# Kernel tuning notes

Hardware: AMD Instinct MI355X
Metric: run time of the kernel (lower is better)

Reference implementation:

```python
import jax, jax.numpy as jnp
import numpy as np
from jax import lax

NUM_CLASSES = 80
NUM_ANCHORS = 5
INPUT_SIZE = 1280
LAYER = 40  # INPUT_SIZE / 32
CONF_T = 0.5
IOU_T = 0.45
ANCHORS = np.array([[1.3221, 1.73145], [3.19275, 4.00944], [5.05587, 8.09892],
                    [9.47112, 4.84053], [11.2364, 10.0071]], dtype=np.float32)


def setup_inputs() -> dict:
    key = jax.random.key(0)
    x = jax.random.normal(key, (1, NUM_ANCHORS * (5 + NUM_CLASSES), LAYER, LAYER), dtype=jnp.float32)
    return {"x": x, "scaled_anchors": jnp.asarray(ANCHORS)}


def _decode(x, anchors):
    # x: (1, A*(5+C), H, W) -> boxes (N,4) in input_size scale, conf (N,), cls (N,)
    b, _, H, W = x.shape
    A = anchors.shape[0]
    stride_w = INPUT_SIZE / W
    stride_h = INPUT_SIZE / H
    pred = x.reshape(b, A, 5 + NUM_CLASSES, H, W).transpose(0, 1, 3, 4, 2)  # (b,A,H,W,5+C)
    gx, gy = jnp.meshgrid(jnp.arange(W, dtype=x.dtype), jnp.arange(H, dtype=x.dtype))
    grid = jnp.stack([gx, gy], axis=-1)  # (H,W,2)
    pxy = jax.nn.sigmoid(pred[..., 0:2]) + grid  # (b,A,H,W,2)
    pwh = jnp.exp(pred[..., 2:4]) * anchors[None, :, None, None, :]
    stride = jnp.array([stride_w, stride_h, stride_w, stride_h], dtype=x.dtype)
    pbox = jnp.concatenate([pxy, pwh], axis=-1) * stride  # (b,A,H,W,4)
    pconf = jax.nn.sigmoid(pred[..., 4])
    # sigmoid is monotonic so argmax over sigmoid(logits) == argmax over logits
    pcls = jnp.argmax(pred[..., 5:], axis=-1)
    N = A * H * W
    return pbox.reshape(N, 4), pconf.reshape(N), pcls.reshape(N)


def _nms_keep(boxes, conf, cls):
    # Greedy per-class NMS; returns fixed-shape boolean keep mask of shape (N,)
    N = boxes.shape[0]
    valid = conf > CONF_T
    cx, cy, w, h = boxes[:, 0], boxes[:, 1], boxes[:, 2], boxes[:, 3]
    x1, y1, x2, y2 = cx - w / 2, cy - h / 2, cx + w / 2, cy + h / 2
    area = jnp.maximum(x2 - x1, 0.0) * jnp.maximum(y2 - y1, 0.0)
    ix1 = jnp.maximum(x1[:, None], x1[None, :])
    iy1 = jnp.maximum(y1[:, None], y1[None, :])
    ix2 = jnp.minimum(x2[:, None], x2[None, :])
    iy2 = jnp.minimum(y2[:, None], y2[None, :])
    inter = jnp.maximum(ix2 - ix1, 0.0) * jnp.maximum(iy2 - iy1, 0.0)
    iou = inter / (area[:, None] + area[None, :] - inter + 1e-9)  # (N,N)

    score = jnp.where(valid, conf, -1.0)
    order = jnp.argsort(-score)

    def step(carry, idx):
        keep, sup = carry
        active = valid[idx] & ~sup[idx]
        keep = keep.at[idx].set(active)
        row = (iou[idx] > IOU_T) & (cls == cls[idx])
        sup = sup | (active & row)
        return (keep, sup), None

    init = (jnp.zeros(N, dtype=bool), jnp.zeros(N, dtype=bool))
    (keep, _), _ = lax.scan(step, init, order)
    return keep


def reference(x, scaled_anchors):
    boxes, conf, cls = _decode(x, scaled_anchors)
    out = jnp.concatenate([boxes, conf[:, None], cls[:, None].astype(boxes.dtype)], axis=-1)  # (N,6)
    keep = _nms_keep(boxes, conf, cls)
    # fixed-shape output: suppressed / low-confidence rows are zeroed, keep mask returned
    return out * keep[:, None].astype(out.dtype), keep
```

## Files before the change

kernel.cpp:

```cpp
#include <hip/hip_runtime.h>

#define NCLS 80
#define NA 5
#define HW 1600
#define GW 40
#define NBOX 8000
#define CONF_THR 0.5f
#define IOU_THR 0.45f
#define STRIDE_F 32.0f
#define CAP 128

#define WS_BX 0
#define WS_BY (NBOX)
#define WS_BW (2*NBOX)
#define WS_BH (3*NBOX)
#define WS_CF (4*NBOX)
#define WS_X1 (5*NBOX)
#define WS_Y1 (6*NBOX)
#define WS_X2 (7*NBOX)
#define WS_Y2 (8*NBOX)
#define WS_CNT (9*NBOX)
#define WS_BCONF (9*NBOX + 128)
#define WS_BIDX  (9*NBOX + 128 + NCLS*CAP)

__device__ __forceinline__ float sigmoidf_(float t) {
  return 1.0f / (1.0f + expf(-t));
}

__global__ void k_zero(float* ws) {
  int t = threadIdx.x;
  if (t < NCLS) ((int*)(ws + WS_CNT))[t] = 0;
}

__global__ void k_decode(const float* __restrict__ x,
                         const float* __restrict__ anchors,
                         float* __restrict__ ws,
                         float* __restrict__ out) {
  int n = blockIdx.x * blockDim.x + threadIdx.x;
  if (n >= NBOX) return;
  int a = n / HW, r = n - a * HW;
  int gi = r / GW, gj = r - gi * GW;
  const float* base = x + (size_t)a * (5 + NCLS) * HW + r;

  float t0 = base[0];
  float t1 = base[HW];
  float t2 = base[2 * HW];
  float t3 = base[3 * HW];
  float t4 = base[4 * HW];
  float ax = anchors[2 * a], ay = anchors[2 * a + 1];

  float cx = (sigmoidf_(t0) + (float)gj) * STRIDE_F;
  float cy = (sigmoidf_(t1) + (float)gi) * STRIDE_F;
  float bw = (expf(t2) * ax) * STRIDE_F;
  float bh = (expf(t3) * ay) * STRIDE_F;
  float cf = sigmoidf_(t4);

  float best = base[5 * HW];
  int bi = 0;
#pragma unroll
  for (int c = 1; c < NCLS; ++c) {
    float v = base[(5 + c) * HW];
    if (v > best) { best = v; bi = c; }
  }

  float x1 = cx - bw * 0.5f, y1 = cy - bh * 0.5f;
  float x2 = cx + bw * 0.5f, y2 = cy + bh * 0.5f;

  ws[WS_BX + n] = cx;  ws[WS_BY + n] = cy;
  ws[WS_BW + n] = bw;  ws[WS_BH + n] = bh;
  ws[WS_CF + n] = cf;
  ws[WS_X1 + n] = x1;  ws[WS_Y1 + n] = y1;
  ws[WS_X2 + n] = x2;  ws[WS_Y2 + n] = y2;

  float* o = out + (size_t)n * 6;
  o[0] = 0.0f; o[1] = 0.0f; o[2] = 0.0f;
  o[3] = 0.0f; o[4] = 0.0f; o[5] = 0.0f;
  out[6 * NBOX + n] = 0.0f;

  if (cf > CONF_THR) {
    int slot = atomicAdd((int*)(ws + WS_CNT) + bi, 1);
    if (slot < CAP) {
      ws[WS_BCONF + bi * CAP + slot] = cf;
      ((int*)(ws + WS_BIDX))[bi * CAP + slot] = n;
    }
  }
}

__global__ void k_nms(const float* __restrict__ ws, float* __restrict__ out) {
  __shared__ float sconf[CAP];
  __shared__ int   sidx[CAP];
  __shared__ int   ssort[CAP];
  __shared__ float sx1[CAP], sy1[CAP], sx2[CAP], sy2[CAP], sar[CAP];

  int c = blockIdx.x, lane = threadIdx.x;
  int n = ((const int*)(ws + WS_CNT))[c];
  if (n > CAP) n = CAP;
  if (n <= 0) return;

  for (int i = lane; i < n; i += 64) {
    sconf[i] = ws[WS_BCONF + c * CAP + i];
    sidx[i]  = ((const int*)(ws + WS_BIDX))[c * CAP + i];
  }
  __syncthreads();

  for (int p = lane; p < n; p += 64) {
    float cp = sconf[p]; int ip = sidx[p]; int rk = 0;
    for (int q = 0; q < n; ++q) {
      float cq = sconf[q]; int iq = sidx[q];
      if (cq > cp || (cq == cp && iq < ip)) ++rk;
    }
    ssort[rk] = ip;
  }
  __syncthreads();

  int   gidx[2] = {-1, -1};
  float gbx[2], gby[2], gbw[2], gbh[2], gcf[2];
  float gx1[2], gy1[2], gx2[2], gy2[2], gar[2];
#pragma unroll
  for (int s = 0; s < 2; ++s) {
    int q = lane + 64 * s;
    gbx[s] = gby[s] = gbw[s] = gbh[s] = gcf[s] = 0.0f;
    gx1[s] = gy1[s] = gx2[s] = gy2[s] = gar[s] = 0.0f;
    if (q < n) {
      int i = ssort[q]; gidx[s] = i;
      gbx[s] = ws[WS_BX + i]; gby[s] = ws[WS_BY + i];
      gbw[s] = ws[WS_BW + i]; gbh[s] = ws[WS_BH + i];
      gcf[s] = ws[WS_CF + i];
      gx1[s] = ws[WS_X1 + i]; gy1[s] = ws[WS_Y1 + i];
      gx2[s] = ws[WS_X2 + i]; gy2[s] = ws[WS_Y2 + i];
      gar[s] = fmaxf(gx2[s] - gx1[s], 0.0f) * fmaxf(gy2[s] - gy1[s], 0.0f);
      sx1[q] = gx1[s]; sy1[q] = gy1[s];
      sx2[q] = gx2[s]; sy2[q] = gy2[s]; sar[q] = gar[s];
    }
  }
  __syncthreads();

  unsigned long long sup0 = 0ull, sup1 = 0ull;
  for (int p = 0; p < n; ++p) {
    unsigned long long bit = (p < 64) ? (sup0 >> p) : (sup1 >> (p - 64));
    if (bit & 1ull) continue;
    float px1 = sx1[p], py1 = sy1[p], px2 = sx2[p], py2 = sy2[p], pa = sar[p];
    bool pr0 = false, pr1 = false;
    {
      int q = lane;
      if (q > p && q < n) {
        float ix1 = fmaxf(px1, gx1[0]), iy1 = fmaxf(py1, gy1[0]);
        float ix2 = fminf(px2, gx2[0]), iy2 = fminf(py2, gy2[0]);
        float inter = fmaxf(ix2 - ix1, 0.0f) * fmaxf(iy2 - iy1, 0.0f);
        float iou = inter / (pa + gar[0] - inter + 1e-9f);
        pr0 = iou > IOU_THR;
      }
      q = lane + 64;
      if (q > p && q < n) {
        float ix1 = fmaxf(px1, gx1[1]), iy1 = fmaxf(py1, gy1[1]);
        float ix2 = fminf(px2, gx2[1]), iy2 = fminf(py2, gy2[1]);
        float inter = fmaxf(ix2 - ix1, 0.0f) * fmaxf(iy2 - iy1, 0.0f);
        float iou = inter / (pa + gar[1] - inter + 1e-9f);
        pr1 = iou > IOU_THR;
      }
    }
    sup0 |= __ballot(pr0);
    sup1 |= __ballot(pr1);
  }

#pragma unroll
  for (int s = 0; s < 2; ++s) {
    int q = lane + 64 * s;
    if (q < n) {
      unsigned long long m = s ? sup1 : sup0;
      if (!((m >> lane) & 1ull)) {
        int i = gidx[s];
        float* o = out + (size_t)i * 6;
        o[0] = gbx[s]; o[1] = gby[s]; o[2] = gbw[s]; o[3] = gbh[s];
        o[4] = gcf[s]; o[5] = (float)c;
        out[6 * NBOX + i] = 1.0f;
      }
    }
  }
}

extern "C" void kernel_launch(void* const* d_in, const int* in_sizes, int n_in,
                              void* d_out, int out_size, void* d_ws, size_t ws_size,
                              hipStream_t stream) {
  const float* x = (const float*)d_in[0];
  const float* anchors = (const float*)d_in[1];
  float* out = (float*)d_out;
  float* ws = (float*)d_ws;

  k_zero<<<1, 128, 0, stream>>>(ws);
  k_decode<<<(NBOX + 255) / 256, 256, 0, stream>>>(x, anchors, ws, out);
  k_nms<<<NCLS, 64, 0, stream>>>(ws, out);
}
```

Baseline: 96.82 us.

## Replace atomic per-class bucketing with per-block ballot compaction, drop zero kernel

Decode now writes each box's class index instead of appending valid boxes to per-class buckets with atomics. Each NMS block scans all 8000 boxes with wave ballots to compact its own class's candidates, so the separate zeroing kernel launch goes away. The ranking tie-break now uses the compacted position, which matches index order because the scan is ordered. Corner coordinates are recomputed in NMS rather than stored, and output zeroing becomes coalesced strided writes. The trade-off is that every class block redundantly reads 64KB of workspace in exchange for one fewer launch and no atomic contention.

```diff
diff --git a/kernel.cpp b/kernel.cpp
--- a/kernel.cpp
+++ b/kernel.cpp
@@ -15,21 +15,10 @@
 #define WS_BW (2*NBOX)
 #define WS_BH (3*NBOX)
 #define WS_CF (4*NBOX)
-#define WS_X1 (5*NBOX)
-#define WS_Y1 (6*NBOX)
-#define WS_X2 (7*NBOX)
-#define WS_Y2 (8*NBOX)
-#define WS_CNT (9*NBOX)
-#define WS_BCONF (9*NBOX + 128)
-#define WS_BIDX  (9*NBOX + 128 + NCLS*CAP)
+#define WS_CLS (5*NBOX)
 
 __device__ __forceinline__ float sigmoidf_(float t) {
   return 1.0f / (1.0f + expf(-t));
-}
-
-__global__ void k_zero(float* ws) {
-  int t = threadIdx.x;
-  if (t < NCLS) ((int*)(ws + WS_CNT))[t] = 0;
 }
 
 __global__ void k_decode(const float* __restrict__ x,
@@ -63,51 +52,47 @@
     if (v > best) { best = v; bi = c; }
   }
 
-  float x1 = cx - bw * 0.5f, y1 = cy - bh * 0.5f;
-  float x2 = cx + bw * 0.5f, y2 = cy + bh * 0.5f;
-
   ws[WS_BX + n] = cx;  ws[WS_BY + n] = cy;
   ws[WS_BW + n] = bw;  ws[WS_BH + n] = bh;
   ws[WS_CF + n] = cf;
-  ws[WS_X1 + n] = x1;  ws[WS_Y1 + n] = y1;
-  ws[WS_X2 + n] = x2;  ws[WS_Y2 + n] = y2;
+  ((int*)(ws + WS_CLS))[n] = bi;
 
-  float* o = out + (size_t)n * 6;
-  o[0] = 0.0f; o[1] = 0.0f; o[2] = 0.0f;
-  o[3] = 0.0f; o[4] = 0.0f; o[5] = 0.0f;
-  out[6 * NBOX + n] = 0.0f;
-
-  if (cf > CONF_THR) {
-    int slot = atomicAdd((int*)(ws + WS_CNT) + bi, 1);
-    if (slot < CAP) {
-      ws[WS_BCONF + bi * CAP + slot] = cf;
-      ((int*)(ws + WS_BIDX))[bi * CAP + slot] = n;
-    }
-  }
+#pragma unroll
+  for (int j = 0; j < 7; ++j) out[j * NBOX + n] = 0.0f;
 }
 
 __global__ void k_nms(const float* __restrict__ ws, float* __restrict__ out) {
   __shared__ float sconf[CAP];
-  __shared__ int   sidx[CAP];
+  __shared__ int   slidx[CAP];
   __shared__ int   ssort[CAP];
   __shared__ float sx1[CAP], sy1[CAP], sx2[CAP], sy2[CAP], sar[CAP];
 
   int c = blockIdx.x, lane = threadIdx.x;
-  int n = ((const int*)(ws + WS_CNT))[c];
-  if (n > CAP) n = CAP;
+  const int*   cls = (const int*)(ws + WS_CLS);
+  const float* cfp = ws + WS_CF;
+
+  int count = 0;
+  for (int base_i = 0; base_i < NBOX; base_i += 64) {
+    int i = base_i + lane;
+    float cfi = cfp[i];
+    int ci = cls[i];
+    bool pred = (cfi > CONF_THR) && (ci == c);
+    unsigned long long bal = __ballot(pred);
+    if (pred) {
+      int pos = count + __popcll(bal & ((1ull << lane) - 1ull));
+      if (pos < CAP) { sconf[pos] = cfi; slidx[pos] = i; }
+    }
+    count += (int)__popcll(bal);
+  }
+  int n = count > CAP ? CAP : count;
+  __syncthreads();
   if (n <= 0) return;
 
-  for (int i = lane; i < n; i += 64) {
-    sconf[i] = ws[WS_BCONF + c * CAP + i];
-    sidx[i]  = ((const int*)(ws + WS_BIDX))[c * CAP + i];
-  }
-  __syncthreads();
-
   for (int p = lane; p < n; p += 64) {
-    float cp = sconf[p]; int ip = sidx[p]; int rk = 0;
+    float cp = sconf[p]; int ip = slidx[p]; int rk = 0;
     for (int q = 0; q < n; ++q) {
-      float cq = sconf[q]; int iq = sidx[q];
-      if (cq > cp || (cq == cp && iq < ip)) ++rk;
+      float cq = sconf[q];
+      if (cq > cp || (cq == cp && q < p)) ++rk;
     }
     ssort[rk] = ip;
   }
@@ -119,15 +104,15 @@
 #pragma unroll
   for (int s = 0; s < 2; ++s) {
     int q = lane + 64 * s;
-    gbx[s] = gby[s] = gbw[s] = gbh[s] = gcf[s] = 0.0f;
     gx1[s] = gy1[s] = gx2[s] = gy2[s] = gar[s] = 0.0f;
     if (q < n) {
       int i = ssort[q]; gidx[s] = i;
-      gbx[s] = ws[WS_BX + i]; gby[s] = ws[WS_BY + i];
-      gbw[s] = ws[WS_BW + i]; gbh[s] = ws[WS_BH + i];
+      float bx = ws[WS_BX + i], by = ws[WS_BY + i];
+      float bw = ws[WS_BW + i], bh = ws[WS_BH + i];
+      gbx[s] = bx; gby[s] = by; gbw[s] = bw; gbh[s] = bh;
       gcf[s] = ws[WS_CF + i];
-      gx1[s] = ws[WS_X1 + i]; gy1[s] = ws[WS_Y1 + i];
-      gx2[s] = ws[WS_X2 + i]; gy2[s] = ws[WS_Y2 + i];
+      gx1[s] = bx - bw * 0.5f; gy1[s] = by - bh * 0.5f;
+      gx2[s] = bx + bw * 0.5f; gy2[s] = by + bh * 0.5f;
       gar[s] = fmaxf(gx2[s] - gx1[s], 0.0f) * fmaxf(gy2[s] - gy1[s], 0.0f);
       sx1[q] = gx1[s]; sy1[q] = gy1[s];
       sx2[q] = gx2[s]; sy2[q] = gy2[s]; sar[q] = gar[s];
@@ -187,7 +172,6 @@
   float* out = (float*)d_out;
   float* ws = (float*)d_ws;
 
-  k_zero<<<1, 128, 0, stream>>>(ws);
   k_decode<<<(NBOX + 255) / 256, 256, 0, stream>>>(x, anchors, ws, out);
   k_nms<<<NCLS, 64, 0, stream>>>(ws, out);
 }
```

Measured after the change: 115.3 us. 19.1% more time.
